# Kernel optimization log

Measured on AMD Instinct MI355X. Metric: run time of the kernel, lower is better.

## Reference

```python
import jax, jax.numpy as jnp
import numpy as np


def setup_inputs() -> dict:
    key = jax.random.key(0)
    T, B, N = 2048, 16, 2048
    spikes = (jax.random.uniform(key, (T, B, N)) < 0.05).astype(jnp.float32)
    return {"input_spikes": spikes, "duration": 100}


def reference(input_spikes, duration):
    # Causal sliding-window (boxcar) sum over the time axis of length `duration`,
    # equivalent to conv1d with a ones kernel and causal padding, then clamp to [0,1].
    # psp[t] = clip( sum_{k=max(0,t-duration+1)}^{t} x[k], 0, 1 )
    T = input_spikes.shape[0]
    c = jnp.cumsum(input_spikes, axis=0)                     # [T, ...]
    pad = [(duration, 0)] + [(0, 0)] * (input_spikes.ndim - 1)
    c_shift = jnp.pad(c, pad)[:T]                            # c[t-duration], 0 for t<duration
    win = c - c_shift
    return jnp.clip(win, 0.0, 1.0)
```

## Files before the change

kernel.cpp:

```cpp
#include <hip/hip_runtime.h>


#define T_TOTAL 2048
#define M_COLS  (16 * 2048)
#define CHUNK   256

__global__ __launch_bounds__(256) void psp_scan_kernel(
    const float* __restrict__ x,
    const int*  __restrict__ dur_p,
    float* __restrict__ out)
{
    const int col = blockIdx.x * blockDim.x + threadIdx.x;
    const int t0  = blockIdx.y * CHUNK;
    const int duration = dur_p[0];

    int last = t0 - duration;

    int tstart = t0 - duration + 1;
    if (tstart < 0) tstart = 0;

    const float* xc = x + col;
    float* oc = out + col;

    for (int t = tstart; t < t0; ++t) {
        float v = xc[t * M_COLS];
        if (v != 0.0f) last = t;
    }

    #pragma unroll 4
    for (int t = t0; t < t0 + CHUNK; ++t) {
        float v = xc[t * M_COLS];
        if (v != 0.0f) last = t;
        oc[t * M_COLS] = (t - last < duration) ? 1.0f : 0.0f;
    }
}

extern "C" void kernel_launch(void* const* d_in, const int* in_sizes, int n_in,
                              void* d_out, int out_size, void* d_ws, size_t ws_size,
                              hipStream_t stream) {
    const float* x     = (const float*)d_in[0];
    const int*   dur_p = (const int*)d_in[1];
    float*       out   = (float*)d_out;

    dim3 grid(M_COLS / 256, T_TOTAL / CHUNK);
    dim3 block(256);
    psp_scan_kernel<<<grid, block, 0, stream>>>(x, dur_p, out);
}
```

Baseline: 452.2 us.

## Batch strided loads per thread and halve time chunk for more parallelism

```diff
diff --git a/kernel.cpp b/kernel.cpp
--- a/kernel.cpp
+++ b/kernel.cpp
@@ -3,9 +3,10 @@
 
 #define T_TOTAL 2048
 #define M_COLS  (16 * 2048)
-#define CHUNK   256
+#define CHUNK   128
+#define BATCH   16
 
-__global__ __launch_bounds__(256) void psp_scan_kernel(
+__global__ __launch_bounds__(256, 8) void psp_scan_kernel(
     const float* __restrict__ x,
     const int*  __restrict__ dur_p,
     float* __restrict__ out)
@@ -15,23 +16,42 @@
     const int duration = dur_p[0];
 
     int last = t0 - duration;
-
     int tstart = t0 - duration + 1;
     if (tstart < 0) tstart = 0;
 
     const float* xc = x + col;
     float* oc = out + col;
 
-    for (int t = tstart; t < t0; ++t) {
-        float v = xc[t * M_COLS];
+    int t = tstart;
+    for (; t + BATCH <= t0; t += BATCH) {
+        float v[BATCH];
+        #pragma unroll
+        for (int i = 0; i < BATCH; ++i) v[i] = xc[(size_t)(t + i) * M_COLS];
+        #pragma unroll
+        for (int i = 0; i < BATCH; ++i) {
+            if (v[i] != 0.0f) last = t + i;
+        }
+    }
+    for (; t < t0; ++t) {
+        float v = xc[(size_t)t * M_COLS];
         if (v != 0.0f) last = t;
     }
 
-    #pragma unroll 4
-    for (int t = t0; t < t0 + CHUNK; ++t) {
-        float v = xc[t * M_COLS];
-        if (v != 0.0f) last = t;
-        oc[t * M_COLS] = (t - last < duration) ? 1.0f : 0.0f;
+    for (int tb = t0; tb < t0 + CHUNK; tb += BATCH) {
+        float v[BATCH];
+        #pragma unroll
+        for (int i = 0; i < BATCH; ++i) v[i] = xc[(size_t)(tb + i) * M_COLS];
+
+        float o[BATCH];
+        #pragma unroll
+        for (int i = 0; i < BATCH; ++i) {
+            const int tt = tb + i;
+            last = (v[i] != 0.0f) ? tt : last;
+            o[i] = (tt - last < duration) ? 1.0f : 0.0f;
+        }
+
+        #pragma unroll
+        for (int i = 0; i < BATCH; ++i) oc[(size_t)(tb + i) * M_COLS] = o[i];
     }
 }
 
```

New measurement: 457.3 us. No clear change (+1.1%).

## Pack spikes into time bitmasks and compute windows via masked ORs

Applied to the files above, without the earlier changes.

```diff
diff --git a/kernel.cpp b/kernel.cpp
--- a/kernel.cpp
+++ b/kernel.cpp
@@ -3,46 +3,73 @@
 
 #define T_TOTAL 2048
 #define M_COLS  (16 * 2048)
-#define CHUNK   256
+#define M4      (M_COLS / 4)
+#define TW      (T_TOTAL / 32)
 
-__global__ __launch_bounds__(256) void psp_scan_kernel(
-    const float* __restrict__ x,
+__global__ __launch_bounds__(256) void pack_bits(
+    const float4* __restrict__ x,
+    uint4* __restrict__ bm)
+{
+    const int c4  = blockIdx.x * 256 + threadIdx.x;
+    const int twb = blockIdx.y;
+
+    unsigned w0 = 0, w1 = 0, w2 = 0, w3 = 0;
+    const float4* xp = x + (size_t)(twb * 32) * M4 + c4;
+    #pragma unroll
+    for (int i = 0; i < 32; ++i) {
+        float4 v = xp[(size_t)i * M4];
+        w0 |= (v.x != 0.0f ? 1u : 0u) << i;
+        w1 |= (v.y != 0.0f ? 1u : 0u) << i;
+        w2 |= (v.z != 0.0f ? 1u : 0u) << i;
+        w3 |= (v.w != 0.0f ? 1u : 0u) << i;
+    }
+    bm[(size_t)twb * M4 + c4] = make_uint4(w0, w1, w2, w3);
+}
+
+#define TB 8
+
+__global__ __launch_bounds__(256) void window_or(
+    const uint4* __restrict__ bm,
     const int*  __restrict__ dur_p,
-    float* __restrict__ out)
+    float4* __restrict__ out)
 {
-    const int col = blockIdx.x * blockDim.x + threadIdx.x;
-    const int t0  = blockIdx.y * CHUNK;
+    const int c4 = blockIdx.x * 256 + threadIdx.x;
+    const int t0 = blockIdx.y * TB;
     const int duration = dur_p[0];
 
-    int last = t0 - duration;
+    #pragma unroll
+    for (int k = 0; k < TB; ++k) {
+        const int t = t0 + k;
+        int L = t - (duration - 1);
+        if (L < 0) L = 0;
+        const int tw = t >> 5, r  = t & 31;
+        const int Lw = L >> 5, Lr = L & 31;
 
-    int tstart = t0 - duration + 1;
-    if (tstart < 0) tstart = 0;
-
-    const float* xc = x + col;
-    float* oc = out + col;
-
-    for (int t = tstart; t < t0; ++t) {
-        float v = xc[t * M_COLS];
-        if (v != 0.0f) last = t;
-    }
-
-    #pragma unroll 4
-    for (int t = t0; t < t0 + CHUNK; ++t) {
-        float v = xc[t * M_COLS];
-        if (v != 0.0f) last = t;
-        oc[t * M_COLS] = (t - last < duration) ? 1.0f : 0.0f;
+        unsigned ax = 0, ay = 0, az = 0, aw = 0;
+        for (int wi = Lw; wi <= tw; ++wi) {
+            unsigned m = 0xffffffffu;
+            if (wi == tw) m &= (2u << r) - 1u;
+            if (wi == Lw) m &= ~((1u << Lr) - 1u);
+            uint4 w = bm[(size_t)wi * M4 + c4];
+            ax |= w.x & m; ay |= w.y & m; az |= w.z & m; aw |= w.w & m;
+        }
+        float4 o;
+        o.x = ax ? 1.0f : 0.0f;
+        o.y = ay ? 1.0f : 0.0f;
+        o.z = az ? 1.0f : 0.0f;
+        o.w = aw ? 1.0f : 0.0f;
+        out[(size_t)t * M4 + c4] = o;
     }
 }
 
 extern "C" void kernel_launch(void* const* d_in, const int* in_sizes, int n_in,
                               void* d_out, int out_size, void* d_ws, size_t ws_size,
                               hipStream_t stream) {
-    const float* x     = (const float*)d_in[0];
-    const int*   dur_p = (const int*)d_in[1];
-    float*       out   = (float*)d_out;
+    const float4* x     = (const float4*)d_in[0];
+    const int*    dur_p = (const int*)d_in[1];
+    float4*       out   = (float4*)d_out;
+    uint4*        bm    = (uint4*)d_ws;
 
-    dim3 grid(M_COLS / 256, T_TOTAL / CHUNK);
-    dim3 block(256);
-    psp_scan_kernel<<<grid, block, 0, stream>>>(x, dur_p, out);
+    pack_bits<<<dim3(M4 / 256, TW), 256, 0, stream>>>(x, bm);
+    window_or<<<dim3(M4 / 256, T_TOTAL / TB), 256, 0, stream>>>(bm, dur_p, out);
 }
```

New measurement: 464.6 us. 1.03x slower.

## Pack spikes into bitmask, then compute window via bitwise OR unpack

Applied to the files above, without the earlier changes.

```diff
diff --git a/kernel.cpp b/kernel.cpp
--- a/kernel.cpp
+++ b/kernel.cpp
@@ -3,46 +3,95 @@
 
 #define T_TOTAL 2048
 #define M_COLS  (16 * 2048)
-#define CHUNK   256
+#define M4      8192
+#define TQ      (T_TOTAL / 8)
+#define GRID    1024
 
-__global__ __launch_bounds__(256) void psp_scan_kernel(
-    const float* __restrict__ x,
-    const int*  __restrict__ dur_p,
+typedef float f32x4 __attribute__((ext_vector_type(4)));
+
+__global__ __launch_bounds__(256) void pack8(
+    const float4* __restrict__ x,
+    unsigned* __restrict__ bm8)
+{
+    const int tid = threadIdx.x;
+    for (int w = blockIdx.x; w < TQ * 32; w += GRID) {
+        const int tq = w >> 5;
+        const int c4 = ((w & 31) << 8) + tid;
+        const float4* xp = x + (size_t)tq * 8 * M4 + c4;
+
+        float4 v[8];
+        #pragma unroll
+        for (int r = 0; r < 8; ++r) v[r] = xp[(size_t)r * M4];
+
+        unsigned s = 0;
+        #pragma unroll
+        for (int r = 0; r < 8; ++r) {
+            s |= (v[r].x != 0.0f ? 1u : 0u) << r;
+            s |= (v[r].y != 0.0f ? 1u : 0u) << (8 + r);
+            s |= (v[r].z != 0.0f ? 1u : 0u) << (16 + r);
+            s |= (v[r].w != 0.0f ? 1u : 0u) << (24 + r);
+        }
+        bm8[(size_t)tq * M4 + c4] = s;
+    }
+}
+
+__global__ __launch_bounds__(256) void unpack_or(
+    const unsigned* __restrict__ bm8,
+    const int* __restrict__ dur_p,
     float* __restrict__ out)
 {
-    const int col = blockIdx.x * blockDim.x + threadIdx.x;
-    const int t0  = blockIdx.y * CHUNK;
     const int duration = dur_p[0];
+    const int tid = threadIdx.x;
 
-    int last = t0 - duration;
+    for (int ci = blockIdx.x; ci < T_TOTAL * 32; ci += GRID) {
+        const int t  = ci >> 5;
+        const int c4 = ((ci & 31) << 8) + tid;
+        int L = t - (duration - 1); if (L < 0) L = 0;
+        const int tq = t >> 3, Lq = L >> 3;
 
-    int tstart = t0 - duration + 1;
-    if (tstart < 0) tstart = 0;
+        unsigned acc = 0;
+        if (tq - Lq <= 13) {
+            unsigned wv[14];
+            #pragma unroll
+            for (int j = 0; j < 14; ++j) {
+                int wi = Lq + j; if (wi > TQ - 1) wi = TQ - 1;
+                wv[j] = bm8[(size_t)wi * M4 + c4];
+            }
+            #pragma unroll
+            for (int j = 0; j < 14; ++j) {
+                const int wi = Lq + j;
+                int lo = L - wi * 8; if (lo < 0) lo = 0;
+                int hi = t - wi * 8; if (hi > 7) hi = 7;
+                unsigned m8 = (hi >= lo) ? (((2u << hi) - 1u) & ~((1u << lo) - 1u)) : 0u;
+                acc |= wv[j] & (m8 * 0x01010101u);
+            }
+        } else {
+            for (int wi = Lq; wi <= tq; ++wi) {
+                int lo = L - wi * 8; if (lo < 0) lo = 0;
+                int hi = t - wi * 8; if (hi > 7) hi = 7;
+                unsigned m8 = (((2u << hi) - 1u) & ~((1u << lo) - 1u));
+                acc |= bm8[(size_t)wi * M4 + c4] & (m8 * 0x01010101u);
+            }
+        }
 
-    const float* xc = x + col;
-    float* oc = out + col;
-
-    for (int t = tstart; t < t0; ++t) {
-        float v = xc[t * M_COLS];
-        if (v != 0.0f) last = t;
-    }
-
-    #pragma unroll 4
-    for (int t = t0; t < t0 + CHUNK; ++t) {
-        float v = xc[t * M_COLS];
-        if (v != 0.0f) last = t;
-        oc[t * M_COLS] = (t - last < duration) ? 1.0f : 0.0f;
+        f32x4 o;
+        o.x = (acc & 0x000000ffu) ? 1.0f : 0.0f;
+        o.y = (acc & 0x0000ff00u) ? 1.0f : 0.0f;
+        o.z = (acc & 0x00ff0000u) ? 1.0f : 0.0f;
+        o.w = (acc & 0xff000000u) ? 1.0f : 0.0f;
+        __builtin_nontemporal_store(
+            o, (f32x4*)(out + (size_t)ci * 1024 + (size_t)tid * 4));
     }
 }
 
 extern "C" void kernel_launch(void* const* d_in, const int* in_sizes, int n_in,
                               void* d_out, int out_size, void* d_ws, size_t ws_size,
                               hipStream_t stream) {
-    const float* x     = (const float*)d_in[0];
-    const int*   dur_p = (const int*)d_in[1];
-    float*       out   = (float*)d_out;
+    const float4* x     = (const float4*)d_in[0];
+    const int*    dur_p = (const int*)d_in[1];
+    float*        out   = (float*)d_out;
+    unsigned*     bm8   = (unsigned*)d_ws;
 
-    dim3 grid(M_COLS / 256, T_TOTAL / CHUNK);
-    dim3 block(256);
-    psp_scan_kernel<<<grid, block, 0, stream>>>(x, dur_p, out);
+    pack8<<<GRID, 256, 0, stream>>>(x, bm8);
+    unpack_or<<<GRID, 256, 0, stream>>>(bm8, dur_p, out);
 }
```

After: 499.7 us. 1.11x slower.
